# Kernel tuning notes

Measured on AMD Instinct MI355X. Metric: run time of the kernel, lower is better.

## Reference

```python
import jax, jax.numpy as jnp
import numpy as np

B, LQ, LK, D = 16, 2048, 2048, 64
EPS = 1e-13
KEEP_PROB = 0.8  # fraction of key positions kept in the mask


def setup_inputs() -> dict:
    key = jax.random.key(0)
    kq, kk, kv, km = jax.random.split(key, 4)
    q = jax.random.normal(kq, (B, LQ, D), dtype=jnp.float32)
    k = jax.random.normal(kk, (B, LK, D), dtype=jnp.float32)
    v = jax.random.normal(kv, (B, LK, D), dtype=jnp.float32)
    # binary 0/1 float mask over key positions (ESIM-style padding mask)
    v_mask = (jax.random.uniform(km, (B, LK)) < KEEP_PROB).astype(jnp.float32)
    return {"q": q, "k": k, "v": v, "v_mask": v_mask}


def masked_softmax(scores, mask):
    # ESIM masked_softmax: softmax(scores * mask) * mask, renormalized.
    m = mask[:, None, :]  # [B, 1, Lk] broadcast over query dim
    p = jax.nn.softmax(scores * m, axis=-1) * m
    return p / (jnp.sum(p, axis=-1, keepdims=True) + EPS)


def reference(q, k, v, v_mask):
    scores = jnp.einsum("bqd,bkd->bqk", q, k)  # [B, Lq, Lk]
    attend = masked_softmax(scores, v_mask)
    return jnp.einsum("bqk,bkd->bqd", attend, v)  # [B, Lq, D]
```

## Files before the change

kernel.cpp:

```cpp
#include <hip/hip_runtime.h>
#include <hip/hip_bf16.h>
#include <stdint.h>

#define NB 16
#define SLQ 2048
#define SLK 2048
#define DD 64
#define BQ 64
#define BK 64
#define NT (SLK / BK)

typedef _Float16 f16x8 __attribute__((ext_vector_type(8)));
typedef short s16x8 __attribute__((ext_vector_type(8)));
typedef float f32x4 __attribute__((ext_vector_type(4)));
typedef float f32x2 __attribute__((ext_vector_type(2)));

typedef __attribute__((address_space(1))) const void gvoid;
typedef __attribute__((address_space(3))) void lvoid;

__device__ __forceinline__ int swzb(int row, int bytecol) {
    return row * 128 + (bytecol ^ ((row & 7) << 4));
}

__device__ __forceinline__ void gload16(const void* g, void* l) {
    __builtin_amdgcn_global_load_lds((gvoid*)g, (lvoid*)l, 16, 0, 0);
}

__device__ __forceinline__ uint16_t f2bf(float f) {
    __bf16 h = (__bf16)f;
    return __builtin_bit_cast(uint16_t, h);
}
__device__ __forceinline__ float bf2f(uint16_t u) {
    uint32_t x = ((uint32_t)u) << 16;
    return __builtin_bit_cast(float, x);
}

__global__ __launch_bounds__(256) void prep_qk(const float* __restrict__ q,
                                               const float* __restrict__ k,
                                               char* __restrict__ qs,
                                               char* __restrict__ ks) {
    const int tl = blockIdx.x & 511;
    const float* src = (blockIdx.x < 512 ? q : k) + (size_t)tl * (BK * DD);
    char* dst = (blockIdx.x < 512 ? qs : ks) + (size_t)tl * (BK * DD * 2);
    #pragma unroll
    for (int it = 0; it < 2; ++it) {
        int c = threadIdx.x + it * 256;
        int row = c >> 3, col8 = c & 7;
        f32x4 a  = *(const f32x4*)(src + row * DD + col8 * 8);
        f32x4 b2 = *(const f32x4*)(src + row * DD + col8 * 8 + 4);
        f16x8 h;
        #pragma unroll
        for (int j = 0; j < 4; ++j) { h[j] = (_Float16)a[j]; h[4 + j] = (_Float16)b2[j]; }
        *(f16x8*)(dst + swzb(row, col8 * 16)) = h;
    }
}

__global__ __launch_bounds__(256) void prep_v(const float* __restrict__ v,
                                              char* __restrict__ vts) {
    const int tl = blockIdx.x;
    const float* src = v + (size_t)tl * (BK * DD);
    char* dst = vts + (size_t)tl * (BK * DD * 2);
    const int d = threadIdx.x & 63;
    #pragma unroll
    for (int it = 0; it < 2; ++it) {
        int key8 = (threadIdx.x >> 6) + it * 4;
        s16x8 h;
        #pragma unroll
        for (int j = 0; j < 8; ++j)
            h[j] = (short)f2bf(src[(key8 * 8 + j) * DD + d]);
        *(s16x8*)(dst + swzb(d, key8 * 16)) = h;
    }
}

__global__ __launch_bounds__(256) void prep_bias(const float* __restrict__ vm,
                                                 float* __restrict__ bias2) {
    int i = blockIdx.x * 256 + threadIdx.x;
    bias2[i] = (vm[i] != 0.f) ? 0.f : -1e30f;
}

__global__ __launch_bounds__(256, 4)
void attn_fwd(const char* __restrict__ qs, const char* __restrict__ ks,
              const char* __restrict__ vts, const float* __restrict__ bias2,
              float* __restrict__ po, float* __restrict__ pl,
              float* __restrict__ out, int ls)
{
    __shared__ __align__(16) char lp[BQ * DD * 2];
    __shared__ __align__(16) char lk[2][BK * DD * 2];
    __shared__ __align__(16) char lv[2][BK * DD * 2];

    const int tid  = threadIdx.x;
    const int lane = tid & 63;
    const int w    = tid >> 6;
    const int lg   = lane >> 4;
    const int lm   = lane & 15;

    const int G = 512 << ls;
    int wg = blockIdx.x;
    wg = (wg & 7) * (G >> 3) + (wg >> 3);
    const int qt = wg & 31;
    const int rest = wg >> 5;
    const int sp = rest & ((1 << ls) - 1);
    const int b  = rest >> ls;
    const int NTE = NT >> ls;

    const char* qtile = qs  + (size_t)(b * 32 + qt) * 8192;
    const char* kbase = ks  + (size_t)(b * 32 + sp * NTE) * 8192;
    const char* vbase = vts + (size_t)(b * 32 + sp * NTE) * 8192;
    const float* mbias = bias2 + (size_t)b * SLK + sp * NTE * BK;

    #pragma unroll
    for (int i = 0; i < 2; ++i) {
        int ch = w * 2 + i;
        gload16(qtile + ch * 1024 + lane * 16, lp + ch * 1024);
    }
    #pragma unroll
    for (int i = 0; i < 2; ++i) {
        int ch = w * 2 + i;
        gload16(kbase + ch * 1024 + lane * 16, lk[0] + ch * 1024);
        gload16(vbase + ch * 1024 + lane * 16, lv[0] + ch * 1024);
    }
    asm volatile("s_waitcnt vmcnt(0)" ::: "memory");
    __syncthreads();

    f16x8 qf[2];
    #pragma unroll
    for (int kc = 0; kc < 2; ++kc)
        qf[kc] = *(const f16x8*)(lp + swzb(w * 16 + lm, kc * 64 + lg * 16));

    s16x8 ones;
    #pragma unroll
    for (int j = 0; j < 8; ++j) ones[j] = (short)0x3F80;

    f32x4 oacc[4], rsacc;
    #pragma unroll
    for (int d = 0; d < 4; ++d) oacc[d] = (f32x4){0.f, 0.f, 0.f, 0.f};
    rsacc = (f32x4){0.f, 0.f, 0.f, 0.f};

    int buf = 0;
    for (int kt = 0; kt < NTE; ++kt) {
        float bv[4];
        #pragma unroll
        for (int f = 0; f < 4; ++f) bv[f] = mbias[kt * BK + f * 16 + lm];

        if (kt + 1 < NTE) {
            const char* kg = kbase + (size_t)(kt + 1) * 8192;
            const char* vg = vbase + (size_t)(kt + 1) * 8192;
            #pragma unroll
            for (int i = 0; i < 2; ++i) {
                int ch = w * 2 + i;
                gload16(kg + ch * 1024 + lane * 16, lk[buf ^ 1] + ch * 1024);
                gload16(vg + ch * 1024 + lane * 16, lv[buf ^ 1] + ch * 1024);
            }
        }

        f32x4 s[4];
        #pragma unroll
        for (int f = 0; f < 4; ++f) s[f] = (f32x4){0.f, 0.f, 0.f, 0.f};
        #pragma unroll
        for (int f = 0; f < 4; ++f) {
            #pragma unroll
            for (int kc = 0; kc < 2; ++kc) {
                f16x8 kf = *(const f16x8*)(lk[buf] + swzb(f * 16 + lm, kc * 64 + lg * 16));
                s[f] = __builtin_amdgcn_mfma_f32_16x16x32_f16(qf[kc], kf, s[f], 0, 0, 0);
            }
        }

        #pragma unroll
        for (int f = 0; f < 4; ++f) {
            #pragma unroll
            for (int i = 0; i < 4; ++i) {
                float p = __expf(s[f][i] + bv[f]);
                *(uint16_t*)(lp + swzb(w * 16 + lg * 4 + i, (f * 16 + lm) * 2)) = f2bf(p);
            }
        }

        #pragma unroll
        for (int kc = 0; kc < 2; ++kc) {
            s16x8 pf = *(const s16x8*)(lp + swzb(w * 16 + lm, kc * 64 + lg * 16));
            rsacc = __builtin_amdgcn_mfma_f32_16x16x32_bf16(pf, ones, rsacc, 0, 0, 0);
            #pragma unroll
            for (int d = 0; d < 4; ++d) {
                s16x8 vf = *(const s16x8*)(lv[buf] + swzb(d * 16 + lm, kc * 64 + lg * 16));
                oacc[d] = __builtin_amdgcn_mfma_f32_16x16x32_bf16(pf, vf, oacc[d], 0, 0, 0);
            }
        }

        asm volatile("s_waitcnt vmcnt(0)" ::: "memory");
        __syncthreads();
        buf ^= 1;
    }

    if (ls == 0) {
        float* ob = out + ((size_t)b * SLQ + (size_t)qt * BQ) * DD;
        #pragma unroll
        for (int i = 0; i < 4; ++i) {
            float inv = 1.f / (rsacc[i] + 1e-13f);
            int row = w * 16 + lg * 4 + i;
            #pragma unroll
            for (int d = 0; d < 4; ++d)
                ob[row * DD + d * 16 + lm] = oacc[d][i] * inv;
        }
    } else {
        float* pob = po + (size_t)wg * (BQ * DD);
        #pragma unroll
        for (int i = 0; i < 4; ++i) {
            int row = w * 16 + lg * 4 + i;
            #pragma unroll
            for (int d = 0; d < 4; ++d)
                pob[row * DD + d * 16 + lm] = oacc[d][i];
            if (lm == 0) pl[(size_t)wg * BQ + row] = rsacc[i];
        }
    }
}

__global__ __launch_bounds__(256)
void merge2(const float* __restrict__ po, const float* __restrict__ pl,
            float* __restrict__ out) {
    const int t  = blockIdx.x;
    const int b  = t >> 5, qt = t & 31;
    const int i0 = b * 64 + qt;
    const int i1 = i0 + 32;
    const int r0 = threadIdx.x >> 4;
    const int c4 = (threadIdx.x & 15) * 4;
    const float* p0 = po + (size_t)i0 * (BQ * DD);
    const float* p1 = po + (size_t)i1 * (BQ * DD);
    float* ob = out + ((size_t)b * SLQ + (size_t)qt * BQ) * DD;
    #pragma unroll
    for (int rr = 0; rr < 64; rr += 16) {
        int r = r0 + rr;
        float l = pl[(size_t)i0 * BQ + r] + pl[(size_t)i1 * BQ + r] + 1e-13f;
        float inv = 1.f / l;
        f32x4 a = *(const f32x4*)(p0 + r * DD + c4);
        f32x4 c = *(const f32x4*)(p1 + r * DD + c4);
        f32x4 o;
        #pragma unroll
        for (int j = 0; j < 4; ++j) o[j] = (a[j] + c[j]) * inv;
        *(f32x4*)(ob + r * DD + c4) = o;
    }
}

__global__ __launch_bounds__(256, 2)
void attn_fallback(const float* __restrict__ q, const float* __restrict__ k,
                   const float* __restrict__ v, const float* __restrict__ vm,
                   float* __restrict__ out)
{
    __shared__ __align__(16) char lqh[BQ * DD * 2];
    __shared__ __align__(16) char lql[BQ * DD * 2];
    __shared__ __align__(16) char lkh[BK * DD * 2];
    __shared__ __align__(16) char lkl[BK * DD * 2];
    __shared__ __align__(16) char lvt[DD * BK * 2];
    __shared__ __align__(16) char lp [BQ * BK * 2];
    __shared__ float lmask[BK];

    const int tid  = threadIdx.x;
    const int lane = tid & 63;
    const int w    = tid >> 6;
    const int lg   = lane >> 4;
    const int lm   = lane & 15;

    const int b  = blockIdx.y;
    const int qt = blockIdx.x;

    const float* qb = q + ((size_t)b * SLQ + (size_t)qt * BQ) * DD;
    const float* kb = k + (size_t)b * SLK * DD;
    const float* vb = v + (size_t)b * SLK * DD;
    const float* mb = vm + (size_t)b * SLK;

    #pragma unroll
    for (int it = 0; it < 2; ++it) {
        int c = tid + it * 256;
        int row = c >> 3, col8 = c & 7;
        f32x4 a  = *(const f32x4*)(qb + row * DD + col8 * 8);
        f32x4 bb = *(const f32x4*)(qb + row * DD + col8 * 8 + 4);
        s16x8 h, l;
        #pragma unroll
        for (int j = 0; j < 4; ++j) {
            uint16_t hh = f2bf(a[j]);
            h[j] = (short)hh; l[j] = (short)f2bf(a[j] - bf2f(hh));
            uint16_t hb = f2bf(bb[j]);
            h[4 + j] = (short)hb; l[4 + j] = (short)f2bf(bb[j] - bf2f(hb));
        }
        *(s16x8*)(lqh + swzb(row, col8 * 16)) = h;
        *(s16x8*)(lql + swzb(row, col8 * 16)) = l;
    }
    __syncthreads();

    s16x8 qfh[2], qfl[2];
    #pragma unroll
    for (int kc = 0; kc < 2; ++kc) {
        qfh[kc] = *(const s16x8*)(lqh + swzb(w * 16 + lm, kc * 64 + lg * 16));
        qfl[kc] = *(const s16x8*)(lql + swzb(w * 16 + lm, kc * 64 + lg * 16));
    }

    float mrow[4], lrow[4];
    f32x4 oacc[4];
    #pragma unroll
    for (int i = 0; i < 4; ++i) { mrow[i] = -1e30f; lrow[i] = 0.f; }
    #pragma unroll
    for (int d = 0; d < 4; ++d) oacc[d] = (f32x4){0.f, 0.f, 0.f, 0.f};

    for (int kt = 0; kt < NT; ++kt) {
        __syncthreads();
        const float* ks2 = kb + (size_t)kt * BK * DD;
        const float* vs = vb + (size_t)kt * BK * DD;

        #pragma unroll
        for (int it = 0; it < 2; ++it) {
            int c = tid + it * 256;
            int row = c >> 3, col8 = c & 7;
            f32x4 a  = *(const f32x4*)(ks2 + row * DD + col8 * 8);
            f32x4 bb = *(const f32x4*)(ks2 + row * DD + col8 * 8 + 4);
            s16x8 h, l;
            #pragma unroll
            for (int j = 0; j < 4; ++j) {
                uint16_t hh = f2bf(a[j]);
                h[j] = (short)hh; l[j] = (short)f2bf(a[j] - bf2f(hh));
                uint16_t hb = f2bf(bb[j]);
                h[4 + j] = (short)hb; l[4 + j] = (short)f2bf(bb[j] - bf2f(hb));
            }
            *(s16x8*)(lkh + swzb(row, col8 * 16)) = h;
            *(s16x8*)(lkl + swzb(row, col8 * 16)) = l;
        }
        #pragma unroll
        for (int it = 0; it < 8; ++it) {
            int c = tid + it * 256;
            int key = c >> 5, dp = (c & 31) * 2;
            f32x2 a = *(const f32x2*)(vs + key * DD + dp);
            *(uint16_t*)(lvt + swzb(dp,     key * 2)) = f2bf(a[0]);
            *(uint16_t*)(lvt + swzb(dp + 1, key * 2)) = f2bf(a[1]);
        }
        if (tid < BK) lmask[tid] = mb[kt * BK + tid];
        __syncthreads();

        f32x4 s[4];
        #pragma unroll
        for (int f = 0; f < 4; ++f) s[f] = (f32x4){0.f, 0.f, 0.f, 0.f};
        #pragma unroll
        for (int f = 0; f < 4; ++f) {
            #pragma unroll
            for (int kc = 0; kc < 2; ++kc) {
                s16x8 kfh = *(const s16x8*)(lkh + swzb(f * 16 + lm, kc * 64 + lg * 16));
                s16x8 kfl = *(const s16x8*)(lkl + swzb(f * 16 + lm, kc * 64 + lg * 16));
                s[f] = __builtin_amdgcn_mfma_f32_16x16x32_bf16(qfh[kc], kfh, s[f], 0, 0, 0);
                s[f] = __builtin_amdgcn_mfma_f32_16x16x32_bf16(qfh[kc], kfl, s[f], 0, 0, 0);
                s[f] = __builtin_amdgcn_mfma_f32_16x16x32_bf16(qfl[kc], kfh, s[f], 0, 0, 0);
            }
        }

        float mv[4];
        #pragma unroll
        for (int f = 0; f < 4; ++f) mv[f] = lmask[f * 16 + lm];

        float pmax[4];
        #pragma unroll
        for (int i = 0; i < 4; ++i) {
            float x = -1e30f;
            #pragma unroll
            for (int f = 0; f < 4; ++f) {
                float sv = (mv[f] != 0.f) ? s[f][i] : -1e30f;
                s[f][i] = sv;
                x = fmaxf(x, sv);
            }
            #pragma unroll
            for (int off = 1; off < 16; off <<= 1)
                x = fmaxf(x, __shfl_xor(x, off, 64));
            pmax[i] = x;
        }

        float scl[4];
        #pragma unroll
        for (int i = 0; i < 4; ++i) {
            float mn = fmaxf(mrow[i], pmax[i]);
            scl[i] = __expf(mrow[i] - mn);
            mrow[i] = mn;
        }
        float rs[4] = {0.f, 0.f, 0.f, 0.f};
        #pragma unroll
        for (int f = 0; f < 4; ++f) {
            #pragma unroll
            for (int i = 0; i < 4; ++i) {
                float p = __expf(s[f][i] - mrow[i]);
                s[f][i] = p;
                rs[i] += p;
            }
        }
        #pragma unroll
        for (int i = 0; i < 4; ++i) {
            #pragma unroll
            for (int off = 1; off < 16; off <<= 1)
                rs[i] += __shfl_xor(rs[i], off, 64);
            lrow[i] = lrow[i] * scl[i] + rs[i];
        }
        #pragma unroll
        for (int d = 0; d < 4; ++d)
            #pragma unroll
            for (int i = 0; i < 4; ++i)
                oacc[d][i] *= scl[i];

        #pragma unroll
        for (int f = 0; f < 4; ++f)
            #pragma unroll
            for (int i = 0; i < 4; ++i)
                *(uint16_t*)(lp + swzb(w * 16 + lg * 4 + i, (f * 16 + lm) * 2)) = f2bf(s[f][i]);
        __syncthreads();

        #pragma unroll
        for (int kc = 0; kc < 2; ++kc) {
            s16x8 pf = *(const s16x8*)(lp + swzb(w * 16 + lm, kc * 64 + lg * 16));
            #pragma unroll
            for (int d = 0; d < 4; ++d) {
                s16x8 vf = *(const s16x8*)(lvt + swzb(d * 16 + lm, kc * 64 + lg * 16));
                oacc[d] = __builtin_amdgcn_mfma_f32_16x16x32_bf16(pf, vf, oacc[d], 0, 0, 0);
            }
        }
    }

    float* ob = out + ((size_t)b * SLQ + (size_t)qt * BQ) * DD;
    #pragma unroll
    for (int i = 0; i < 4; ++i) {
        float inv = 1.f / (lrow[i] + 1e-13f);
        int row = w * 16 + lg * 4 + i;
        #pragma unroll
        for (int d = 0; d < 4; ++d)
            ob[row * DD + d * 16 + lm] = oacc[d][i] * inv;
    }
}

extern "C" void kernel_launch(void* const* d_in, const int* in_sizes, int n_in,
                              void* d_out, int out_size, void* d_ws, size_t ws_size,
                              hipStream_t stream) {
    const float* q  = (const float*)d_in[0];
    const float* k  = (const float*)d_in[1];
    const float* v  = (const float*)d_in[2];
    const float* vm = (const float*)d_in[3];
    float* out = (float*)d_out;

    const size_t TB   = (size_t)NB * SLK * DD * 2;
    const size_t BIAS = (size_t)NB * SLK * 4;
    const size_t PL   = (size_t)1024 * BQ * 4;
    const size_t PO   = (size_t)1024 * BQ * DD * 4;
    const size_t need_min   = 3 * TB + BIAS;
    const size_t need_split = need_min + PL + PO;

    if (ws_size < need_min) {
        dim3 grid(SLQ / BQ, NB);
        attn_fallback<<<grid, dim3(256), 0, stream>>>(q, k, v, vm, out);
        return;
    }

    char*  qs    = (char*)d_ws;
    char*  ks    = qs + TB;
    char*  vts   = ks + TB;
    float* bias2 = (float*)(vts + TB);
    float* pl    = (float*)((char*)bias2 + BIAS);
    float* po    = (float*)((char*)pl + PL);

    const int ls = (ws_size >= need_split) ? 1 : 0;

    prep_qk  <<<dim3(1024), dim3(256), 0, stream>>>(q, k, qs, ks);
    prep_v   <<<dim3(512),  dim3(256), 0, stream>>>(v, vts);
    prep_bias<<<dim3(NB * SLK / 256), dim3(256), 0, stream>>>(vm, bias2);
    attn_fwd <<<dim3(512 << ls), dim3(256), 0, stream>>>(qs, ks, vts, bias2, po, pl, out, ls);
    if (ls == 1)
        merge2<<<dim3(512), dim3(256), 0, stream>>>(po, pl, out);
}
```

Baseline: 53.66 us.

## Use 128-row Q tiles with 32x32 MFMA, fuse prep kernels, generalize key split

Doubles the query tile to 128 rows, with each wave owning 32 rows, and switches from 16x16 to 32x32x16 MFMA instructions. This raises reuse of each K/V tile loaded into LDS. The three prep kernels are merged into one launch, and Q is prescaled by log2(e) so the softmax can use exp2f. The key-dimension split now allows up to 3 parts based on workspace size, with a generic merge kernel. The trade-offs are fewer workgroups, an occupancy hint lowered to 3, and more accumulator registers.

```diff
diff --git a/kernel.cpp b/kernel.cpp
--- a/kernel.cpp
+++ b/kernel.cpp
@@ -6,20 +6,26 @@
 #define SLQ 2048
 #define SLK 2048
 #define DD 64
-#define BQ 64
+#define BQ 128
 #define BK 64
 #define NT (SLK / BK)
+#define QTILES (SLQ / BQ)
+#define LOG2E 1.44269504f
 
 typedef _Float16 f16x8 __attribute__((ext_vector_type(8)));
 typedef short s16x8 __attribute__((ext_vector_type(8)));
 typedef float f32x4 __attribute__((ext_vector_type(4)));
 typedef float f32x2 __attribute__((ext_vector_type(2)));
+typedef float f32x16 __attribute__((ext_vector_type(16)));
 
 typedef __attribute__((address_space(1))) const void gvoid;
 typedef __attribute__((address_space(3))) void lvoid;
 
 __device__ __forceinline__ int swzb(int row, int bytecol) {
     return row * 128 + (bytecol ^ ((row & 7) << 4));
+}
+__device__ __forceinline__ int ldsq(int row, int bytecol) {
+    return (row >> 6) * 8192 + swzb(row & 63, bytecol);
 }
 
 __device__ __forceinline__ void gload16(const void* g, void* l) {
@@ -35,58 +41,223 @@
     return __builtin_bit_cast(float, x);
 }
 
-__global__ __launch_bounds__(256) void prep_qk(const float* __restrict__ q,
-                                               const float* __restrict__ k,
-                                               char* __restrict__ qs,
-                                               char* __restrict__ ks) {
-    const int tl = blockIdx.x & 511;
-    const float* src = (blockIdx.x < 512 ? q : k) + (size_t)tl * (BK * DD);
-    char* dst = (blockIdx.x < 512 ? qs : ks) + (size_t)tl * (BK * DD * 2);
-    #pragma unroll
-    for (int it = 0; it < 2; ++it) {
-        int c = threadIdx.x + it * 256;
-        int row = c >> 3, col8 = c & 7;
-        f32x4 a  = *(const f32x4*)(src + row * DD + col8 * 8);
-        f32x4 b2 = *(const f32x4*)(src + row * DD + col8 * 8 + 4);
-        f16x8 h;
-        #pragma unroll
-        for (int j = 0; j < 4; ++j) { h[j] = (_Float16)a[j]; h[4 + j] = (_Float16)b2[j]; }
-        *(f16x8*)(dst + swzb(row, col8 * 16)) = h;
-    }
-}
-
-__global__ __launch_bounds__(256) void prep_v(const float* __restrict__ v,
-                                              char* __restrict__ vts) {
-    const int tl = blockIdx.x;
-    const float* src = v + (size_t)tl * (BK * DD);
-    char* dst = vts + (size_t)tl * (BK * DD * 2);
-    const int d = threadIdx.x & 63;
-    #pragma unroll
-    for (int it = 0; it < 2; ++it) {
-        int key8 = (threadIdx.x >> 6) + it * 4;
-        s16x8 h;
-        #pragma unroll
-        for (int j = 0; j < 8; ++j)
-            h[j] = (short)f2bf(src[(key8 * 8 + j) * DD + d]);
-        *(s16x8*)(dst + swzb(d, key8 * 16)) = h;
-    }
-}
-
-__global__ __launch_bounds__(256) void prep_bias(const float* __restrict__ vm,
-                                                 float* __restrict__ bias2) {
-    int i = blockIdx.x * 256 + threadIdx.x;
-    bias2[i] = (vm[i] != 0.f) ? 0.f : -1e30f;
-}
-
-__global__ __launch_bounds__(256, 4)
+__global__ __launch_bounds__(256)
+void prep_all(const float* __restrict__ q, const float* __restrict__ k,
+              const float* __restrict__ v, const float* __restrict__ vm,
+              char* __restrict__ qs, char* __restrict__ ks,
+              char* __restrict__ vts, float* __restrict__ bias2) {
+    const int bid = blockIdx.x;
+    if (bid < 1024) {
+        const int tl = bid & 511;
+        const bool isq = bid < 512;
+        const float sc = isq ? LOG2E : 1.0f;
+        const float* src = (isq ? q : k) + (size_t)tl * (BK * DD);
+        char* dst = (isq ? qs : ks) + (size_t)tl * (BK * DD * 2);
+        #pragma unroll
+        for (int it = 0; it < 2; ++it) {
+            int c = threadIdx.x + it * 256;
+            int row = c >> 3, col8 = c & 7;
+            f32x4 a  = *(const f32x4*)(src + row * DD + col8 * 8);
+            f32x4 b2 = *(const f32x4*)(src + row * DD + col8 * 8 + 4);
+            f16x8 h;
+            #pragma unroll
+            for (int j = 0; j < 4; ++j) {
+                h[j] = (_Float16)(a[j] * sc);
+                h[4 + j] = (_Float16)(b2[j] * sc);
+            }
+            *(f16x8*)(dst + swzb(row, col8 * 16)) = h;
+        }
+    } else if (bid < 1536) {
+        const int tl = bid - 1024;
+        const float* src = v + (size_t)tl * (BK * DD);
+        char* dst = vts + (size_t)tl * (BK * DD * 2);
+        const int d = threadIdx.x & 63;
+        #pragma unroll
+        for (int it = 0; it < 2; ++it) {
+            int key8 = (threadIdx.x >> 6) + it * 4;
+            s16x8 h;
+            #pragma unroll
+            for (int j = 0; j < 8; ++j)
+                h[j] = (short)f2bf(src[(key8 * 8 + j) * DD + d]);
+            *(s16x8*)(dst + swzb(d, key8 * 16)) = h;
+        }
+    } else {
+        int i = (bid - 1536) * 256 + threadIdx.x;
+        bias2[i] = (vm[i] != 0.f) ? 0.f : -2e30f;
+    }
+}
+
+__global__ __launch_bounds__(256, 3)
 void attn_fwd(const char* __restrict__ qs, const char* __restrict__ ks,
               const char* __restrict__ vts, const float* __restrict__ bias2,
               float* __restrict__ po, float* __restrict__ pl,
-              float* __restrict__ out, int ls)
+              float* __restrict__ out, int nsp)
 {
     __shared__ __align__(16) char lp[BQ * DD * 2];
     __shared__ __align__(16) char lk[2][BK * DD * 2];
     __shared__ __align__(16) char lv[2][BK * DD * 2];
+
+    const int tid  = threadIdx.x;
+    const int lane = tid & 63;
+    const int w    = tid >> 6;
+    const int lh   = lane >> 5;
+    const int lr   = lane & 31;
+
+    const int G = 256 * nsp;
+    int wg = blockIdx.x;
+    wg = (wg & 7) * (G >> 3) + (wg >> 3);
+    const int qt   = wg & 15;
+    const int rest = wg >> 4;
+    const int sp   = rest % nsp;
+    const int b    = rest / nsp;
+
+    const int qq = NT / nsp, rm = NT % nsp;
+    const int t0  = sp * qq + (sp < rm ? sp : rm);
+    const int cnt = qq + (sp < rm ? 1 : 0);
+
+    const char* qtile = qs  + (size_t)(b * 32 + qt * 2) * 8192;
+    const char* kbase = ks  + (size_t)(b * 32 + t0) * 8192;
+    const char* vbase = vts + (size_t)(b * 32 + t0) * 8192;
+    const float* mbias = bias2 + (size_t)b * SLK + t0 * BK;
+
+    #pragma unroll
+    for (int i = 0; i < 4; ++i) {
+        int ch = w * 4 + i;
+        gload16(qtile + ch * 1024 + lane * 16, lp + ch * 1024);
+    }
+    #pragma unroll
+    for (int i = 0; i < 2; ++i) {
+        int ch = w * 2 + i;
+        gload16(kbase + ch * 1024 + lane * 16, lk[0] + ch * 1024);
+        gload16(vbase + ch * 1024 + lane * 16, lv[0] + ch * 1024);
+    }
+    asm volatile("s_waitcnt vmcnt(0)" ::: "memory");
+    __syncthreads();
+
+    f16x8 qf[4];
+    #pragma unroll
+    for (int kd = 0; kd < 4; ++kd)
+        qf[kd] = *(const f16x8*)(lp + ldsq(w * 32 + lr, kd * 32 + lh * 16));
+
+    s16x8 ones;
+    #pragma unroll
+    for (int j = 0; j < 8; ++j) ones[j] = (short)0x3F80;
+
+    f32x16 oacc0 = (f32x16)(0.0f), oacc1 = (f32x16)(0.0f), rsacc = (f32x16)(0.0f);
+
+    int buf = 0;
+    for (int kt = 0; kt < cnt; ++kt) {
+        float bv0 = mbias[kt * BK + lr];
+        float bv1 = mbias[kt * BK + 32 + lr];
+
+        if (kt + 1 < cnt) {
+            const char* kg = kbase + (size_t)(kt + 1) * 8192;
+            const char* vg = vbase + (size_t)(kt + 1) * 8192;
+            #pragma unroll
+            for (int i = 0; i < 2; ++i) {
+                int ch = w * 2 + i;
+                gload16(kg + ch * 1024 + lane * 16, lk[buf ^ 1] + ch * 1024);
+                gload16(vg + ch * 1024 + lane * 16, lv[buf ^ 1] + ch * 1024);
+            }
+        }
+
+        f32x16 s0 = (f32x16)(0.0f), s1 = (f32x16)(0.0f);
+        #pragma unroll
+        for (int kd = 0; kd < 4; ++kd) {
+            f16x8 kf0 = *(const f16x8*)(lk[buf] + swzb(lr,      kd * 32 + lh * 16));
+            f16x8 kf1 = *(const f16x8*)(lk[buf] + swzb(32 + lr, kd * 32 + lh * 16));
+            s0 = __builtin_amdgcn_mfma_f32_32x32x16_f16(qf[kd], kf0, s0, 0, 0, 0);
+            s1 = __builtin_amdgcn_mfma_f32_32x32x16_f16(qf[kd], kf1, s1, 0, 0, 0);
+        }
+
+        #pragma unroll
+        for (int r = 0; r < 16; ++r) {
+            int row = w * 32 + (r & 3) + 8 * (r >> 2) + 4 * lh;
+            float p0 = exp2f(s0[r] + bv0);
+            float p1 = exp2f(s1[r] + bv1);
+            *(uint16_t*)(lp + ldsq(row, lr * 2))      = f2bf(p0);
+            *(uint16_t*)(lp + ldsq(row, 64 + lr * 2)) = f2bf(p1);
+        }
+
+        s16x8 pa[4];
+        #pragma unroll
+        for (int kk = 0; kk < 4; ++kk) {
+            pa[kk] = *(const s16x8*)(lp + ldsq(w * 32 + lr, kk * 32 + lh * 16));
+            rsacc = __builtin_amdgcn_mfma_f32_32x32x16_bf16(pa[kk], ones, rsacc, 0, 0, 0);
+        }
+        #pragma unroll
+        for (int kk = 0; kk < 4; ++kk) {
+            s16x8 vf0 = *(const s16x8*)(lv[buf] + swzb(lr,      kk * 32 + lh * 16));
+            s16x8 vf1 = *(const s16x8*)(lv[buf] + swzb(32 + lr, kk * 32 + lh * 16));
+            oacc0 = __builtin_amdgcn_mfma_f32_32x32x16_bf16(pa[kk], vf0, oacc0, 0, 0, 0);
+            oacc1 = __builtin_amdgcn_mfma_f32_32x32x16_bf16(pa[kk], vf1, oacc1, 0, 0, 0);
+        }
+
+        asm volatile("s_waitcnt vmcnt(0)" ::: "memory");
+        __syncthreads();
+        buf ^= 1;
+    }
+
+    if (nsp == 1) {
+        float* ob = out + ((size_t)b * SLQ + (size_t)qt * BQ) * DD;
+        #pragma unroll
+        for (int r = 0; r < 16; ++r) {
+            int row = w * 32 + (r & 3) + 8 * (r >> 2) + 4 * lh;
+            float inv = 1.f / (rsacc[r] + 1e-13f);
+            ob[row * DD + lr]      = oacc0[r] * inv;
+            ob[row * DD + 32 + lr] = oacc1[r] * inv;
+        }
+    } else {
+        float* pob = po + (size_t)wg * (BQ * DD);
+        #pragma unroll
+        for (int r = 0; r < 16; ++r) {
+            int row = w * 32 + (r & 3) + 8 * (r >> 2) + 4 * lh;
+            pob[row * DD + lr]      = oacc0[r];
+            pob[row * DD + 32 + lr] = oacc1[r];
+            if (lr == 0) pl[(size_t)wg * BQ + row] = rsacc[r];
+        }
+    }
+}
+
+__global__ __launch_bounds__(256)
+void merge_k(const float* __restrict__ po, const float* __restrict__ pl,
+             float* __restrict__ out, int nsp) {
+    const int t  = blockIdx.x;
+    const int b  = t >> 4, qt = t & 15;
+    const int i0 = (b * nsp) * 16 + qt;
+    const int r0 = threadIdx.x >> 4;
+    const int c4 = (threadIdx.x & 15) * 4;
+    float* ob = out + ((size_t)b * SLQ + (size_t)qt * BQ) * DD;
+    for (int rr = 0; rr < BQ; rr += 16) {
+        int r = r0 + rr;
+        float l = 1e-13f;
+        f32x4 acc = (f32x4){0.f, 0.f, 0.f, 0.f};
+        for (int s = 0; s < nsp; ++s) {
+            int idx = i0 + s * 16;
+            l += pl[(size_t)idx * BQ + r];
+            f32x4 a = *(const f32x4*)(po + (size_t)idx * (BQ * DD) + r * DD + c4);
+            acc += a;
+        }
+        float inv = 1.f / l;
+        f32x4 o;
+        #pragma unroll
+        for (int j = 0; j < 4; ++j) o[j] = acc[j] * inv;
+        *(f32x4*)(ob + r * DD + c4) = o;
+    }
+}
+
+__global__ __launch_bounds__(256, 2)
+void attn_fallback(const float* __restrict__ q, const float* __restrict__ k,
+                   const float* __restrict__ v, const float* __restrict__ vm,
+                   float* __restrict__ out)
+{
+    __shared__ __align__(16) char lqh[64 * DD * 2];
+    __shared__ __align__(16) char lql[64 * DD * 2];
+    __shared__ __align__(16) char lkh[BK * DD * 2];
+    __shared__ __align__(16) char lkl[BK * DD * 2];
+    __shared__ __align__(16) char lvt[DD * BK * 2];
+    __shared__ __align__(16) char lpp[64 * BK * 2];
+    __shared__ float lmask[BK];
 
     const int tid  = threadIdx.x;
     const int lane = tid & 63;
@@ -94,174 +265,10 @@
     const int lg   = lane >> 4;
     const int lm   = lane & 15;
 
-    const int G = 512 << ls;
-    int wg = blockIdx.x;
-    wg = (wg & 7) * (G >> 3) + (wg >> 3);
-    const int qt = wg & 31;
-    const int rest = wg >> 5;
-    const int sp = rest & ((1 << ls) - 1);
-    const int b  = rest >> ls;
-    const int NTE = NT >> ls;
-
-    const char* qtile = qs  + (size_t)(b * 32 + qt) * 8192;
-    const char* kbase = ks  + (size_t)(b * 32 + sp * NTE) * 8192;
-    const char* vbase = vts + (size_t)(b * 32 + sp * NTE) * 8192;
-    const float* mbias = bias2 + (size_t)b * SLK + sp * NTE * BK;
-
-    #pragma unroll
-    for (int i = 0; i < 2; ++i) {
-        int ch = w * 2 + i;
-        gload16(qtile + ch * 1024 + lane * 16, lp + ch * 1024);
-    }
-    #pragma unroll
-    for (int i = 0; i < 2; ++i) {
-        int ch = w * 2 + i;
-        gload16(kbase + ch * 1024 + lane * 16, lk[0] + ch * 1024);
-        gload16(vbase + ch * 1024 + lane * 16, lv[0] + ch * 1024);
-    }
-    asm volatile("s_waitcnt vmcnt(0)" ::: "memory");
-    __syncthreads();
-
-    f16x8 qf[2];
-    #pragma unroll
-    for (int kc = 0; kc < 2; ++kc)
-        qf[kc] = *(const f16x8*)(lp + swzb(w * 16 + lm, kc * 64 + lg * 16));
-
-    s16x8 ones;
-    #pragma unroll
-    for (int j = 0; j < 8; ++j) ones[j] = (short)0x3F80;
-
-    f32x4 oacc[4], rsacc;
-    #pragma unroll
-    for (int d = 0; d < 4; ++d) oacc[d] = (f32x4){0.f, 0.f, 0.f, 0.f};
-    rsacc = (f32x4){0.f, 0.f, 0.f, 0.f};
-
-    int buf = 0;
-    for (int kt = 0; kt < NTE; ++kt) {
-        float bv[4];
-        #pragma unroll
-        for (int f = 0; f < 4; ++f) bv[f] = mbias[kt * BK + f * 16 + lm];
-
-        if (kt + 1 < NTE) {
-            const char* kg = kbase + (size_t)(kt + 1) * 8192;
-            const char* vg = vbase + (size_t)(kt + 1) * 8192;
-            #pragma unroll
-            for (int i = 0; i < 2; ++i) {
-                int ch = w * 2 + i;
-                gload16(kg + ch * 1024 + lane * 16, lk[buf ^ 1] + ch * 1024);
-                gload16(vg + ch * 1024 + lane * 16, lv[buf ^ 1] + ch * 1024);
-            }
-        }
-
-        f32x4 s[4];
-        #pragma unroll
-        for (int f = 0; f < 4; ++f) s[f] = (f32x4){0.f, 0.f, 0.f, 0.f};
-        #pragma unroll
-        for (int f = 0; f < 4; ++f) {
-            #pragma unroll
-            for (int kc = 0; kc < 2; ++kc) {
-                f16x8 kf = *(const f16x8*)(lk[buf] + swzb(f * 16 + lm, kc * 64 + lg * 16));
-                s[f] = __builtin_amdgcn_mfma_f32_16x16x32_f16(qf[kc], kf, s[f], 0, 0, 0);
-            }
-        }
-
-        #pragma unroll
-        for (int f = 0; f < 4; ++f) {
-            #pragma unroll
-            for (int i = 0; i < 4; ++i) {
-                float p = __expf(s[f][i] + bv[f]);
-                *(uint16_t*)(lp + swzb(w * 16 + lg * 4 + i, (f * 16 + lm) * 2)) = f2bf(p);
-            }
-        }
-
-        #pragma unroll
-        for (int kc = 0; kc < 2; ++kc) {
-            s16x8 pf = *(const s16x8*)(lp + swzb(w * 16 + lm, kc * 64 + lg * 16));
-            rsacc = __builtin_amdgcn_mfma_f32_16x16x32_bf16(pf, ones, rsacc, 0, 0, 0);
-            #pragma unroll
-            for (int d = 0; d < 4; ++d) {
-                s16x8 vf = *(const s16x8*)(lv[buf] + swzb(d * 16 + lm, kc * 64 + lg * 16));
-                oacc[d] = __builtin_amdgcn_mfma_f32_16x16x32_bf16(pf, vf, oacc[d], 0, 0, 0);
-            }
-        }
-
-        asm volatile("s_waitcnt vmcnt(0)" ::: "memory");
-        __syncthreads();
-        buf ^= 1;
-    }
-
-    if (ls == 0) {
-        float* ob = out + ((size_t)b * SLQ + (size_t)qt * BQ) * DD;
-        #pragma unroll
-        for (int i = 0; i < 4; ++i) {
-            float inv = 1.f / (rsacc[i] + 1e-13f);
-            int row = w * 16 + lg * 4 + i;
-            #pragma unroll
-            for (int d = 0; d < 4; ++d)
-                ob[row * DD + d * 16 + lm] = oacc[d][i] * inv;
-        }
-    } else {
-        float* pob = po + (size_t)wg * (BQ * DD);
-        #pragma unroll
-        for (int i = 0; i < 4; ++i) {
-            int row = w * 16 + lg * 4 + i;
-            #pragma unroll
-            for (int d = 0; d < 4; ++d)
-                pob[row * DD + d * 16 + lm] = oacc[d][i];
-            if (lm == 0) pl[(size_t)wg * BQ + row] = rsacc[i];
-        }
-    }
-}
-
-__global__ __launch_bounds__(256)
-void merge2(const float* __restrict__ po, const float* __restrict__ pl,
-            float* __restrict__ out) {
-    const int t  = blockIdx.x;
-    const int b  = t >> 5, qt = t & 31;
-    const int i0 = b * 64 + qt;
-    const int i1 = i0 + 32;
-    const int r0 = threadIdx.x >> 4;
-    const int c4 = (threadIdx.x & 15) * 4;
-    const float* p0 = po + (size_t)i0 * (BQ * DD);
-    const float* p1 = po + (size_t)i1 * (BQ * DD);
-    float* ob = out + ((size_t)b * SLQ + (size_t)qt * BQ) * DD;
-    #pragma unroll
-    for (int rr = 0; rr < 64; rr += 16) {
-        int r = r0 + rr;
-        float l = pl[(size_t)i0 * BQ + r] + pl[(size_t)i1 * BQ + r] + 1e-13f;
-        float inv = 1.f / l;
-        f32x4 a = *(const f32x4*)(p0 + r * DD + c4);
-        f32x4 c = *(const f32x4*)(p1 + r * DD + c4);
-        f32x4 o;
-        #pragma unroll
-        for (int j = 0; j < 4; ++j) o[j] = (a[j] + c[j]) * inv;
-        *(f32x4*)(ob + r * DD + c4) = o;
-    }
-}
-
-__global__ __launch_bounds__(256, 2)
-void attn_fallback(const float* __restrict__ q, const float* __restrict__ k,
-                   const float* __restrict__ v, const float* __restrict__ vm,
-                   float* __restrict__ out)
-{
-    __shared__ __align__(16) char lqh[BQ * DD * 2];
-    __shared__ __align__(16) char lql[BQ * DD * 2];
-    __shared__ __align__(16) char lkh[BK * DD * 2];
-    __shared__ __align__(16) char lkl[BK * DD * 2];
-    __shared__ __align__(16) char lvt[DD * BK * 2];
-    __shared__ __align__(16) char lp [BQ * BK * 2];
-    __shared__ float lmask[BK];
-
-    const int tid  = threadIdx.x;
-    const int lane = tid & 63;
-    const int w    = tid >> 6;
-    const int lg   = lane >> 4;
-    const int lm   = lane & 15;
-
     const int b  = blockIdx.y;
     const int qt = blockIdx.x;
 
-    const float* qb = q + ((size_t)b * SLQ + (size_t)qt * BQ) * DD;
+    const float* qb = q + ((size_t)b * SLQ + (size_t)qt * 64) * DD;
     const float* kb = k + (size_t)b * SLK * DD;
     const float* vb = v + (size_t)b * SLK * DD;
     const float* mb = vm + (size_t)b * SLK;
@@ -401,12 +408,12 @@
         for (int f = 0; f < 4; ++f)
             #pragma unroll
             for (int i = 0; i < 4; ++i)
-                *(uint16_t*)(lp + swzb(w * 16 + lg * 4 + i, (f * 16 + lm) * 2)) = f2bf(s[f][i]);
+                *(uint16_t*)(lpp + swzb(w * 16 + lg * 4 + i, (f * 16 + lm) * 2)) = f2bf(s[f][i]);
         __syncthreads();
 
         #pragma unroll
         for (int kc = 0; kc < 2; ++kc) {
-            s16x8 pf = *(const s16x8*)(lp + swzb(w * 16 + lm, kc * 64 + lg * 16));
+            s16x8 pf = *(const s16x8*)(lpp + swzb(w * 16 + lm, kc * 64 + lg * 16));
             #pragma unroll
             for (int d = 0; d < 4; ++d) {
                 s16x8 vf = *(const s16x8*)(lvt + swzb(d * 16 + lm, kc * 64 + lg * 16));
@@ -415,7 +422,7 @@
         }
     }
 
-    float* ob = out + ((size_t)b * SLQ + (size_t)qt * BQ) * DD;
+    float* ob = out + ((size_t)b * SLQ + (size_t)qt * 64) * DD;
     #pragma unroll
     for (int i = 0; i < 4; ++i) {
         float inv = 1.f / (lrow[i] + 1e-13f);
@@ -435,17 +442,23 @@
     const float* vm = (const float*)d_in[3];
     float* out = (float*)d_out;
 
-    const size_t TB   = (size_t)NB * SLK * DD * 2;
-    const size_t BIAS = (size_t)NB * SLK * 4;
-    const size_t PL   = (size_t)1024 * BQ * 4;
-    const size_t PO   = (size_t)1024 * BQ * DD * 4;
-    const size_t need_min   = 3 * TB + BIAS;
-    const size_t need_split = need_min + PL + PO;
-
-    if (ws_size < need_min) {
-        dim3 grid(SLQ / BQ, NB);
-        attn_fallback<<<grid, dim3(256), 0, stream>>>(q, k, v, vm, out);
-        return;
+    const size_t TB     = (size_t)NB * SLK * DD * 2;
+    const size_t BIAS   = (size_t)NB * SLK * 4;
+    const size_t PL_PER = (size_t)NB * QTILES * BQ * 4;
+    const size_t PO_PER = (size_t)NB * QTILES * BQ * DD * 4;
+    const size_t base = 3 * TB + BIAS;
+
+    int nsp = 0;
+    for (int c = 3; c >= 1; --c) {
+        if (ws_size >= base + (size_t)c * (PL_PER + PO_PER)) { nsp = c; break; }
+    }
+    if (nsp == 0) {
+        if (ws_size >= base) nsp = 1;
+        else {
+            dim3 grid(SLQ / 64, NB);
+            attn_fallback<<<grid, dim3(256), 0, stream>>>(q, k, v, vm, out);
+            return;
+        }
     }
 
     char*  qs    = (char*)d_ws;
@@ -453,14 +466,10 @@
     char*  vts   = ks + TB;
     float* bias2 = (float*)(vts + TB);
     float* pl    = (float*)((char*)bias2 + BIAS);
-    float* po    = (float*)((char*)pl + PL);
-
-    const int ls = (ws_size >= need_split) ? 1 : 0;
-
-    prep_qk  <<<dim3(1024), dim3(256), 0, stream>>>(q, k, qs, ks);
-    prep_v   <<<dim3(512),  dim3(256), 0, stream>>>(v, vts);
-    prep_bias<<<dim3(NB * SLK / 256), dim3(256), 0, stream>>>(vm, bias2);
-    attn_fwd <<<dim3(512 << ls), dim3(256), 0, stream>>>(qs, ks, vts, bias2, po, pl, out, ls);
-    if (ls == 1)
-        merge2<<<dim3(512), dim3(256), 0, stream>>>(po, pl, out);
-}
+    float* po    = (float*)((char*)pl + (size_t)nsp * PL_PER);
+
+    prep_all<<<dim3(1664), dim3(256), 0, stream>>>(q, k, v, vm, qs, ks, vts, bias2);
+    attn_fwd<<<dim3(256 * nsp), dim3(256), 0, stream>>>(qs, ks, vts, bias2, po, pl, out, nsp);
+    if (nsp > 1)
+        merge_k<<<dim3(NB * QTILES), dim3(256), 0, stream>>>(po, pl, out, nsp);
+}
```

Measured after the change: 56.16 us. +4.7%, slower.
